# Kernel optimization log

Measured on AMD Instinct MI355X. Metric: run time of the kernel, lower is better.

Reference implementation:

```python
import jax, jax.numpy as jnp
import numpy as np

DIM = 512
HEADS = 8
LANDMARKS = 64


def setup_inputs() -> dict:
    key = jax.random.key(0)
    ks = jax.random.split(key, 9)
    B, N, C = 2, 16384, DIM
    s = 0.02
    return {
        "x": jax.random.normal(ks[0], (B, N, C), dtype=jnp.float32),
        "wq": jax.random.normal(ks[1], (C, C), dtype=jnp.float32) * s,
        "bq": jnp.zeros((C,), dtype=jnp.float32),
        "wk": jax.random.normal(ks[2], (C, C), dtype=jnp.float32) * s,
        "bk": jnp.zeros((C,), dtype=jnp.float32),
        "wv": jax.random.normal(ks[3], (C, C), dtype=jnp.float32) * s,
        "bv": jnp.zeros((C,), dtype=jnp.float32),
        "wo": jax.random.normal(ks[4], (C, C), dtype=jnp.float32) * s,
        "bo": jnp.zeros((C,), dtype=jnp.float32),
    }


def _to_heads(x, H):
    B, N, C = x.shape
    return x.reshape(B, N, H, C // H).transpose(0, 2, 1, 3)  # (B,H,N,hd)


def reference(x, wq, bq, wk, bk, wv, bv, wo, bo):
    B, N, C = x.shape
    H = HEADS
    hd = C // H
    scale = hd ** (-0.5)
    m = min(LANDMARKS, N)

    q = _to_heads(x @ wq.T + bq, H) * scale  # (B,H,N,hd)
    k = _to_heads(x @ wk.T + bk, H)
    v = _to_heads(x @ wv.T + bv, H)

    if N <= m * 2:
        attn = jax.nn.softmax(jnp.einsum("bhnd,bhkd->bhnk", q, k), axis=-1)
        out = jnp.einsum("bhnk,bhkd->bhnd", attn, v)
    else:
        seg = (N + m - 1) // m
        pad = seg * m - N
        if pad > 0:
            q_p = jnp.pad(q, ((0, 0), (0, 0), (0, pad), (0, 0)))
            k_p = jnp.pad(k, ((0, 0), (0, 0), (0, pad), (0, 0)))
        else:
            q_p, k_p = q, k
        # landmarks: mean over consecutive segments of length seg (zero-pad included, as in torch)
        q_land = q_p.reshape(B, H, m, seg, hd).mean(3)  # (B,H,m,hd)
        k_land = k_p.reshape(B, H, m, seg, hd).mean(3)

        ker1 = jax.nn.softmax(jnp.einsum("bhnd,bhmd->bhnm", q, k_land), axis=-1)  # (B,H,N,m)
        ker2 = jax.nn.softmax(jnp.einsum("bhld,bhmd->bhlm", q_land, k_land), axis=-1)  # (B,H,m,m)
        ker3 = jax.nn.softmax(jnp.einsum("bhmd,bhnd->bhmn", q_land, k), axis=-1)  # (B,H,m,N)
        ker2_inv = jnp.linalg.pinv(ker2)  # (B,H,m,m)

        kv = jnp.einsum("bhmn,bhnd->bhmd", ker3, v)  # (B,H,m,hd)
        out = jnp.einsum("bhnm,bhmd->bhnd", ker1, ker2_inv @ kv)

    out = out.transpose(0, 2, 1, 3).reshape(B, N, C)
    return out @ wo.T + bo
```

## Files before the change

### kernel.cpp

```cpp
#include <hip/hip_runtime.h>
#include <stdint.h>


constexpr int B_   = 2;
constexpr int N_   = 16384;
constexpr int C_   = 512;
constexpr int H_   = 8;
constexpr int HD_  = 64;
constexpr int LM_  = 64;
constexpr int SEG_ = 256;
constexpr int BH_  = 16;
constexpr int NCH_ = 16;
constexpr int NPART_ = 64;
constexpr int SW1_ = 4;
constexpr int SW2_ = 1;

#define RCOND_ (640.0 * 1.1920928955078125e-07)

typedef unsigned short ushort4_t __attribute__((ext_vector_type(4)));
typedef unsigned short ushort8_t __attribute__((ext_vector_type(8)));
typedef __bf16 bf16x8 __attribute__((ext_vector_type(8)));
typedef float f32x4 __attribute__((ext_vector_type(4)));

__device__ inline float bf2f(unsigned short u) {
  union { unsigned int i; float f; } x; x.i = ((unsigned int)u) << 16; return x.f;
}
__device__ inline unsigned short f2bf(float f) {
  union { float f; unsigned int i; } x; x.f = f;
  unsigned int lsb = (x.i >> 16) & 1;
  return (unsigned short)((x.i + 0x7fffu + lsb) >> 16);
}
__device__ inline bf16x8 ld_bf8(const unsigned short* p) { return *(const bf16x8*)p; }

__device__ __forceinline__ void gload_lds16(const unsigned short* gsrc, unsigned short* ldst) {
  __builtin_amdgcn_global_load_lds((const __attribute__((address_space(1))) void*)gsrc,
                                   (__attribute__((address_space(3))) void*)ldst, 16, 0, 0);
}

__global__ __launch_bounds__(256) void cvt_w4_kernel(const float* __restrict__ wq,
                                                     const float* __restrict__ wk,
                                                     const float* __restrict__ wv,
                                                     const float* __restrict__ wo,
                                                     unsigned short* __restrict__ dq,
                                                     unsigned short* __restrict__ dk,
                                                     unsigned short* __restrict__ dv,
                                                     unsigned short* __restrict__ dwo) {
  int which = blockIdx.y;
  const float* src = which == 0 ? wq : which == 1 ? wk : which == 2 ? wv : wo;
  unsigned short* dst = which == 0 ? dq : which == 1 ? dk : which == 2 ? dv : dwo;
  int i = blockIdx.x * 256 + threadIdx.x;
  const float* s = src + (size_t)i * 8;
  float4 x0 = *(const float4*)(s);
  float4 x1 = *(const float4*)(s + 4);
  ushort8_t u;
  u[0] = f2bf(x0.x); u[1] = f2bf(x0.y); u[2] = f2bf(x0.z); u[3] = f2bf(x0.w);
  u[4] = f2bf(x1.x); u[5] = f2bf(x1.y); u[6] = f2bf(x1.z); u[7] = f2bf(x1.w);
  *(ushort8_t*)(dst + (size_t)i * 8) = u;
}

__global__ __launch_bounds__(256) void seg_mean_kernel(const float* __restrict__ x,
                                                       float* __restrict__ xbar,
                                                       unsigned short* __restrict__ xb) {
  int bl = blockIdx.x;
  int b = bl / LM_, l = bl % LM_;
  int t = threadIdx.x;
  int c4 = t & 127;
  int rh = t >> 7;
  const size_t rowbase = (size_t)b * N_ + (size_t)l * SEG_;
  const float* xp = x + rowbase * C_;
  float4 s = make_float4(0.f, 0.f, 0.f, 0.f);
  for (int r = rh * 128; r < rh * 128 + 128; ++r) {
    float4 v = *(const float4*)(xp + (size_t)r * C_ + c4 * 4);
    s.x += v.x; s.y += v.y; s.z += v.z; s.w += v.w;
    ushort4_t u;
    u[0] = f2bf(v.x); u[1] = f2bf(v.y); u[2] = f2bf(v.z); u[3] = f2bf(v.w);
    *(ushort4_t*)(xb + (rowbase + r) * C_ + c4 * 4) = u;
  }
  __shared__ float red[2][512];
  *(float4*)&red[rh][c4 * 4] = s;
  __syncthreads();
  if (rh == 0) {
    float4 a = *(float4*)&red[0][c4 * 4];
    float4 c = *(float4*)&red[1][c4 * 4];
    const float invs = 1.0f / SEG_;
    float4 o;
    o.x = (a.x + c.x) * invs; o.y = (a.y + c.y) * invs;
    o.z = (a.z + c.z) * invs; o.w = (a.w + c.w) * invs;
    *(float4*)(xbar + (size_t)bl * C_ + c4 * 4) = o;
  }
}

__global__ __launch_bounds__(256) void land_gemm_kernel(const float* __restrict__ xbar,
                                                        const float* __restrict__ wq,
                                                        const float* __restrict__ bq,
                                                        const float* __restrict__ wk,
                                                        const float* __restrict__ bk,
                                                        float* __restrict__ qland,
                                                        float* __restrict__ kland,
                                                        unsigned short* __restrict__ qlbh,
                                                        unsigned short* __restrict__ qlbl,
                                                        unsigned short* __restrict__ klb) {
  __shared__ float As[32][68];
  __shared__ float Ws[32][68];
  int which = blockIdx.x >> 1;
  int row0 = (blockIdx.x & 1) * 64;
  int col0 = blockIdx.y * 64;
  const float* A = xbar;
  const float* W = which ? wk : wq;
  const float* bias = which ? bk : bq;
  float scale = which ? 1.0f : 0.125f;
  float* out = which ? kland : qland;
  int tid = threadIdx.x;
  int tm = tid >> 4, tn = tid & 15;
  float acc[4][4] = {};
  for (int k0 = 0; k0 < C_; k0 += 32) {
#pragma unroll
    for (int i = 0; i < 2; ++i) {
      int s = tid + i * 256;
      int r = s >> 3;
      int kg = (s & 7) << 2;
      float4 av = *(const float4*)(A + (size_t)(row0 + r) * C_ + k0 + kg);
      As[kg + 0][r] = av.x; As[kg + 1][r] = av.y;
      As[kg + 2][r] = av.z; As[kg + 3][r] = av.w;
      float4 wv = *(const float4*)(W + (size_t)(col0 + r) * C_ + k0 + kg);
      Ws[kg + 0][r] = wv.x; Ws[kg + 1][r] = wv.y;
      Ws[kg + 2][r] = wv.z; Ws[kg + 3][r] = wv.w;
    }
    __syncthreads();
#pragma unroll
    for (int kk = 0; kk < 32; ++kk) {
      float4 a = *(const float4*)&As[kk][tm * 4];
      float4 b = *(const float4*)&Ws[kk][tn * 4];
      float av[4] = {a.x, a.y, a.z, a.w};
      float bv[4] = {b.x, b.y, b.z, b.w};
#pragma unroll
      for (int i = 0; i < 4; ++i)
#pragma unroll
        for (int j = 0; j < 4; ++j) acc[i][j] += av[i] * bv[j];
    }
    __syncthreads();
  }
#pragma unroll
  for (int i = 0; i < 4; ++i) {
    int row = row0 + tm * 4 + i;
    int d0 = tn * 4;
    float o4[4];
#pragma unroll
    for (int j = 0; j < 4; ++j) o4[j] = (acc[i][j] + bias[col0 + d0 + j]) * scale;
    int b = row / LM_, n = row % LM_;
    int h = col0 >> 6;
    size_t idx = (((size_t)(b * H_ + h) * LM_) + n) * HD_ + d0;
    float4 o; o.x = o4[0]; o.y = o4[1]; o.z = o4[2]; o.w = o4[3];
    *(float4*)(out + idx) = o;
    if (which == 0) {
      ushort4_t uh, ul;
#pragma unroll
      for (int j = 0; j < 4; ++j) {
        unsigned short hbits = f2bf(o4[j]);
        uh[j] = hbits;
        ul[j] = f2bf(o4[j] - bf2f(hbits));
      }
      *(ushort4_t*)(qlbh + idx) = uh;
      *(ushort4_t*)(qlbl + idx) = ul;
    } else {
      ushort4_t uk;
#pragma unroll
      for (int j = 0; j < 4; ++j) uk[j] = f2bf(o4[j]);
      *(ushort4_t*)(klb + idx) = uk;
    }
  }
}

__device__ __forceinline__ void dma_gemm_body(const unsigned short* __restrict__ A,
                                              const unsigned short* __restrict__ W,
                                              const float* __restrict__ bias,
                                              void* __restrict__ out,
                                              float scale, int omode,
                                              int row0, int col0,
                                              unsigned short* Xs, unsigned short* Wl,
                                              int tid) {
  int w = tid >> 6, lane = tid & 63;
  int wr = w >> 1, wc = w & 1;
  f32x4 acc[4][4] = {};

  for (int k0 = 0; k0 < C_; k0 += 32) {
    __syncthreads();
#pragma unroll
    for (int i = 0; i < 2; ++i) {
      const unsigned short* gx = A + (size_t)(row0 + w * 32 + i * 16 + (lane >> 2)) * C_ + k0 + (lane & 3) * 8;
      gload_lds16(gx, &Xs[(w * 32 + i * 16) * 32]);
      const unsigned short* gw = W + (size_t)(col0 + w * 32 + i * 16 + (lane >> 2)) * C_ + k0 + (lane & 3) * 8;
      gload_lds16(gw, &Wl[(w * 32 + i * 16) * 32]);
    }
    __syncthreads();
    bf16x8 af[4], bfr[4];
#pragma unroll
    for (int m = 0; m < 4; ++m)
      af[m] = *(bf16x8*)&Xs[(wr * 64 + m * 16 + (lane & 15)) * 32 + (lane >> 4) * 8];
#pragma unroll
    for (int n = 0; n < 4; ++n)
      bfr[n] = *(bf16x8*)&Wl[(wc * 64 + n * 16 + (lane & 15)) * 32 + (lane >> 4) * 8];
#pragma unroll
    for (int m = 0; m < 4; ++m)
#pragma unroll
      for (int n = 0; n < 4; ++n)
        acc[m][n] = __builtin_amdgcn_mfma_f32_16x16x32_bf16(af[m], bfr[n], acc[m][n], 0, 0, 0);
  }

#pragma unroll
  for (int m = 0; m < 4; ++m) {
    int rbase = row0 + wr * 64 + m * 16 + (lane >> 4) * 4;
#pragma unroll
    for (int n = 0; n < 4; ++n) {
      int c = col0 + wc * 64 + n * 16 + (lane & 15);
      float bc = bias[c];
      if (omode == 0) {
#pragma unroll
        for (int rg = 0; rg < 4; ++rg)
          ((float*)out)[(size_t)(rbase + rg) * C_ + c] = acc[m][n][rg] + bc;
      } else if (omode == 2) {
        int b = rbase >> 14, nn = rbase & 16383;
        int h = c >> 6, d = c & 63;
        ushort4_t u;
#pragma unroll
        for (int rg = 0; rg < 4; ++rg) u[rg] = f2bf((acc[m][n][rg] + bc) * scale);
        *(ushort4_t*)((unsigned short*)out + ((size_t)(b * H_ + h) * HD_ + d) * N_ + nn) = u;
      } else {
#pragma unroll
        for (int rg = 0; rg < 4; ++rg) {
          float val = (acc[m][n][rg] + bc) * scale;
          int r = rbase + rg;
          int b = r >> 14, nn = r & 16383, h = c >> 6, d = c & 63;
          ((unsigned short*)out)[(((size_t)(b * H_ + h) * N_) + nn) * HD_ + d] = f2bf(val);
        }
      }
    }
  }
}

template <int NW>
__device__ __forceinline__ void svd_sweeps(float* a, float* v, char* smemraw,
                                           int w, int lane, int nsweeps) {
  constexpr int RP = 64 / NW;
  float (*Ac)[68] = (float(*)[68])(smemraw);
  float (*Vc)[68] = (float(*)[68])(smemraw + 17408);
  float (*pg)[NW][64] = (float(*)[NW][64])(smemraw + 34816);
  float (*pa)[64] = (float(*)[64])(smemraw + 34816 + 2 * NW * 64 * 4);
  const int r0 = w * RP;
#pragma unroll
  for (int c = 0; c < RP; c += 4) {
    *(float4*)&Ac[lane][r0 + c] = make_float4(a[c], a[c + 1], a[c + 2], a[c + 3]);
    *(float4*)&Vc[lane][r0 + c] = make_float4(v[c], v[c + 1], v[c + 2], v[c + 3]);
  }

  for (int sweep = 0; sweep < nsweeps; ++sweep) {
    float p0 = 0.f, p1 = 0.f;
#pragma unroll
    for (int k = 0; k < RP; k += 2) { p0 = fmaf(a[k], a[k], p0); p1 = fmaf(a[k + 1], a[k + 1], p1); }
    pa[w][lane] = p0 + p1;
    __syncthreads();
    float alpha;
    if constexpr (NW == 4)
      alpha = (pa[0][lane] + pa[1][lane]) + (pa[2][lane] + pa[3][lane]);
    else
      alpha = ((pa[0][lane] + pa[1][lane]) + (pa[2][lane] + pa[3][lane])) +
              ((pa[4][lane] + pa[5][lane]) + (pa[6][lane] + pa[7][lane]));
    for (int mask = 1; mask < 64; ++mask) {
      int buf = mask & 1;
      int partner = lane ^ mask;
      bool lower = lane < partner;
      float beta = __shfl_xor(alpha, mask);
      float o[RP];
#pragma unroll
      for (int c = 0; c < RP; c += 4) {
        float4 t4 = *(float4*)&Ac[partner][r0 + c];
        o[c] = t4.x; o[c + 1] = t4.y; o[c + 2] = t4.z; o[c + 3] = t4.w;
      }
      float g0 = 0.f, g1 = 0.f;
#pragma unroll
      for (int k = 0; k < RP; k += 2) { g0 = fmaf(a[k], o[k], g0); g1 = fmaf(a[k + 1], o[k + 1], g1); }
      pg[buf][w][lane] = g0 + g1;
      __syncthreads();
      float gamma;
      if constexpr (NW == 4)
        gamma = (pg[buf][0][lane] + pg[buf][1][lane]) + (pg[buf][2][lane] + pg[buf][3][lane]);
      else
        gamma = ((pg[buf][0][lane] + pg[buf][1][lane]) + (pg[buf][2][lane] + pg[buf][3][lane])) +
                ((pg[buf][4][lane] + pg[buf][5][lane]) + (pg[buf][6][lane] + pg[buf][7][lane]));
      bool need = (gamma * gamma > 1e-12f * alpha * beta);
      if (__any(need)) {
        float ov[RP];
#pragma unroll
        for (int c = 0; c < RP; c += 4) {
          float4 t4 = *(float4*)&Vc[partner][r0 + c];
          ov[c] = t4.x; ov[c + 1] = t4.y; ov[c + 2] = t4.z; ov[c + 3] = t4.w;
        }
        float ap = lower ? alpha : beta;
        float aq = lower ? beta : alpha;
        float c = 1.f, s = 0.f;
        if (need) {
          float tau = (aq - ap) / (2.f * gamma);
          float t = copysignf(1.f, tau) / (fabsf(tau) + sqrtf(fmaf(tau, tau, 1.f)));
          c = rsqrtf(fmaf(t, t, 1.f));
          s = t * c;
        }
        float sm = lower ? -s : s;
#pragma unroll
        for (int k = 0; k < RP; ++k) a[k] = fmaf(sm, o[k], c * a[k]);
#pragma unroll
        for (int k = 0; k < RP; ++k) v[k] = fmaf(sm, ov[k], c * v[k]);
        float twocsg = 2.f * c * s * gamma;
        alpha = fmaf(c * c, alpha, fmaf(s * s, beta, lower ? -twocsg : twocsg));
#pragma unroll
        for (int cc = 0; cc < RP; cc += 4) {
          *(float4*)&Ac[lane][r0 + cc] = make_float4(a[cc], a[cc + 1], a[cc + 2], a[cc + 3]);
          *(float4*)&Vc[lane][r0 + cc] = make_float4(v[cc], v[cc + 1], v[cc + 2], v[cc + 3]);
        }
      }
    }
  }
}

__device__ void svd_phase1(const float* __restrict__ qland, const float* __restrict__ kland,
                           float* __restrict__ asave, float* __restrict__ vsave,
                           int bh, char* smemraw, int tid) {
  __builtin_amdgcn_s_setprio(3);
  float (*qlS)[65] = (float(*)[65])(smemraw);
  float (*klS)[65] = (float(*)[65])(smemraw + 16640);
  for (int i = 0; i < 2; ++i) {
    int s = tid + i * 512;
    int r = s >> 4, d4 = (s & 15) << 2;
    *(float4*)&qlS[r][d4] = *(const float4*)(qland + ((size_t)bh * 64 + r) * 64 + d4);
    *(float4*)&klS[r][d4] = *(const float4*)(kland + ((size_t)bh * 64 + r) * 64 + d4);
  }
  __syncthreads();
  int w = tid >> 6, lane = tid & 63;
  float a[8], v[8];
#pragma unroll
  for (int k = 0; k < 8; ++k) {
    int row = w * 8 + k;
    float acc = 0.f;
#pragma unroll
    for (int d4 = 0; d4 < 64; d4 += 4) {
      float4 qv = *(float4*)&qlS[row][d4];
      float4 kv = *(float4*)&klS[lane][d4];
      acc += qv.x * kv.x + qv.y * kv.y + qv.z * kv.z + qv.w * kv.w;
    }
    float e = expf(acc);
    float rs = e;
#pragma unroll
    for (int m = 1; m < 64; m <<= 1) rs += __shfl_xor(rs, m);
    a[k] = e * (1.f / rs);
  }
#pragma unroll
  for (int k = 0; k < 8; ++k) v[k] = (w * 8 + k == lane) ? 1.f : 0.f;
  __syncthreads();
  svd_sweeps<8>(a, v, smemraw, w, lane, SW1_);
#pragma unroll
  for (int k = 0; k < 8; ++k) {
    asave[((size_t)bh * 64 + w * 8 + k) * 64 + lane] = a[k];
    vsave[((size_t)bh * 64 + w * 8 + k) * 64 + lane] = v[k];
  }
  __builtin_amdgcn_s_setprio(0);
}

__device__ void svd_phase2(const float* __restrict__ asave, const float* __restrict__ vsave,
                           float* __restrict__ pinv, int bh, char* smemraw, int tid) {
  __builtin_amdgcn_s_setprio(3);
  double (*ps2)[64]  = (double(*)[64])(smemraw + 37888);
  float (*vsL)[65]   = (float(*)[65])(smemraw);
  float (*wasL)[65]  = (float(*)[65])(smemraw + 16640);
  int w = tid >> 6, lane = tid & 63;
  float a[16], v[16];
#pragma unroll
  for (int k = 0; k < 16; ++k) {
    a[k] = asave[((size_t)bh * 64 + w * 16 + k) * 64 + lane];
    v[k] = vsave[((size_t)bh * 64 + w * 16 + k) * 64 + lane];
  }
  svd_sweeps<4>(a, v, smemraw, w, lane, SW2_);

  double psig = 0.0;
#pragma unroll
  for (int k = 0; k < 16; ++k) psig += (double)a[k] * (double)a[k];
  ps2[w][lane] = psig;
  __syncthreads();
  double sig2 = (ps2[0][lane] + ps2[1][lane]) + (ps2[2][lane] + ps2[3][lane]);
  double smax = sig2;
#pragma unroll
  for (int m = 1; m < 64; m <<= 1) smax = fmax(smax, __shfl_xor(smax, m));
  double cutoff2 = smax * (RCOND_ * RCOND_);
  float wgt = (sig2 > cutoff2) ? (float)(1.0 / sig2) : 0.f;

#pragma unroll
  for (int k = 0; k < 16; ++k) {
    vsL[lane][w * 16 + k] = v[k];
    wasL[lane][w * 16 + k] = wgt * a[k];
  }
  __syncthreads();
  int i = tid >> 2;
  int j0 = (tid & 3) * 16;
  float acc[16] = {};
  for (int r = 0; r < 64; ++r) {
    float vv = vsL[r][i];
#pragma unroll
    for (int jj = 0; jj < 16; ++jj) acc[jj] = fmaf(vv, wasL[r][j0 + jj], acc[jj]);
  }
#pragma unroll
  for (int jj = 0; jj < 16; jj += 4) {
    float4 ovv = make_float4(acc[jj], acc[jj + 1], acc[jj + 2], acc[jj + 3]);
    *(float4*)(pinv + ((size_t)bh * 64 + i) * 64 + j0 + jj) = ovv;
  }
  __builtin_amdgcn_s_setprio(0);
}

__global__ __launch_bounds__(512) void fused1_kernel(
    const unsigned short* __restrict__ xb,
    const unsigned short* __restrict__ wqb, const float* __restrict__ bq,
    const unsigned short* __restrict__ wkb, const float* __restrict__ bk,
    const unsigned short* __restrict__ wvb, const float* __restrict__ bv,
    unsigned short* __restrict__ q4, unsigned short* __restrict__ k4,
    unsigned short* __restrict__ vt,
    const float* __restrict__ qland, const float* __restrict__ kland,
    float* __restrict__ asave, float* __restrict__ vsave) {
  __shared__ __align__(16) char smem[40960];
  int tid = threadIdx.x;
  int blk = blockIdx.x;
  if (blk < 16) { svd_phase1(qland, kland, asave, vsave, blk, smem, tid); return; }
  int g = blk - 16;
  int which = g >> 9;
  int subpair = g & 511;
  int half = tid >> 8;
  int ltid = tid & 255;
  int sub = subpair * 2 + half;
  int row0 = (sub >> 2) * 128;
  int col0 = (sub & 3) * 128;
  unsigned short* Xs = (unsigned short*)(smem + half * 16384);
  unsigned short* Wl = Xs + 128 * 32;
  if (which == 0)
    dma_gemm_body(xb, wqb, bq, q4, 0.125f, 1, row0, col0, Xs, Wl, ltid);
  else if (which == 1)
    dma_gemm_body(xb, wkb, bk, k4, 1.0f, 1, row0, col0, Xs, Wl, ltid);
  else
    dma_gemm_body(xb, wvb, bv, vt, 1.0f, 2, row0, col0, Xs, Wl, ltid);
}

__device__ void ker3kv_body(const unsigned short* __restrict__ qlh,
                            const unsigned short* __restrict__ qll,
                            const unsigned short* __restrict__ k4,
                            const unsigned short* __restrict__ vt,
                            float* __restrict__ pacc,
                            float* __restrict__ pacc0,
                            float* __restrict__ ps,
                            int bh, int ch, char* smemraw, int tid) {
  int w = tid >> 6, lane = tid & 63;
  int part = ch * 4 + w;
  int lrow = lane & 15, lgrp = lane >> 4;
  unsigned short* myP = (unsigned short*)smemraw + w * 64 * 72;

  bf16x8 qah[4][2], qal[4][2];
#pragma unroll
  for (int mf = 0; mf < 4; ++mf)
#pragma unroll
    for (int ks = 0; ks < 2; ++ks) {
      size_t off = ((size_t)bh * 64 + mf * 16 + lrow) * 64 + ks * 32 + lgrp * 8;
      qah[mf][ks] = ld_bf8(qlh + off);
      qal[mf][ks] = ld_bf8(qll + off);
    }
  bf16x8 onesf;
#pragma unroll
  for (int j = 0; j < 8; ++j) onesf[j] = (__bf16)1.0f;

  f32x4 kvacc[4][4] = {};
  f32x4 oneacc[4] = {};
  f32x4 ssum[4] = {};

  for (int sub = 0; sub < 4; ++sub) {
    int n0 = ch * 1024 + w * 256 + sub * 64;
    f32x4 sacc[4][4] = {};
#pragma unroll
    for (int ks = 0; ks < 2; ++ks) {
#pragma unroll
      for (int nf = 0; nf < 4; ++nf) {
        bf16x8 kb = ld_bf8(k4 + ((size_t)bh * N_ + n0 + nf * 16 + lrow) * 64 + ks * 32 + lgrp * 8);
#pragma unroll
        for (int mf = 0; mf < 4; ++mf) {
          sacc[mf][nf] = __builtin_amdgcn_mfma_f32_16x16x32_bf16(qah[mf][ks], kb, sacc[mf][nf], 0, 0, 0);
          sacc[mf][nf] = __builtin_amdgcn_mfma_f32_16x16x32_bf16(qal[mf][ks], kb, sacc[mf][nf], 0, 0, 0);
        }
      }
    }
#pragma unroll
    for (int mf = 0; mf < 4; ++mf) {
#pragma unroll
      for (int nf = 0; nf < 4; ++nf) {
#pragma unroll
        for (int r = 0; r < 4; ++r) {
          float pd = expf(sacc[mf][nf][r]) - 1.0f;
          ssum[mf][r] += pd;
          myP[(mf * 16 + lgrp * 4 + r) * 72 + nf * 16 + lrow] = f2bf(pd);
        }
      }
    }
#pragma unroll
    for (int ks = 0; ks < 2; ++ks) {
      bf16x8 pa[4];
#pragma unroll
      for (int mf = 0; mf < 4; ++mf)
        pa[mf] = ld_bf8(myP + (mf * 16 + lrow) * 72 + ks * 32 + lgrp * 8);
#pragma unroll
      for (int nf = 0; nf < 4; ++nf) {
        bf16x8 vb = ld_bf8(vt + ((size_t)bh * 64 + nf * 16 + lrow) * N_ + n0 + ks * 32 + lgrp * 8);
#pragma unroll
        for (int mf = 0; mf < 4; ++mf)
          kvacc[mf][nf] = __builtin_amdgcn_mfma_f32_16x16x32_bf16(pa[mf], vb, kvacc[mf][nf], 0, 0, 0);
        oneacc[nf] = __builtin_amdgcn_mfma_f32_16x16x32_bf16(onesf, vb, oneacc[nf], 0, 0, 0);
      }
    }
  }
#pragma unroll
  for (int mf = 0; mf < 4; ++mf)
#pragma unroll
    for (int m = 1; m < 16; m <<= 1)
#pragma unroll
      for (int r = 0; r < 4; ++r) ssum[mf][r] += __shfl_xor(ssum[mf][r], m);

  size_t pb = (((size_t)bh * NPART_ + part) * 64) * 64;
#pragma unroll
  for (int mf = 0; mf < 4; ++mf)
#pragma unroll
    for (int nf = 0; nf < 4; ++nf)
#pragma unroll
      for (int r = 0; r < 4; ++r)
        pacc[pb + (size_t)(mf * 16 + lgrp * 4 + r) * 64 + nf * 16 + lrow] = kvacc[mf][nf][r];
  if (lrow == 0) {
#pragma unroll
    for (int mf = 0; mf < 4; ++mf)
#pragma unroll
      for (int r = 0; r < 4; ++r)
        ps[((size_t)bh * NPART_ + part) * 64 + mf * 16 + lgrp * 4 + r] = ssum[mf][r];
  }
  if (lgrp == 0) {
#pragma unroll
    for (int nf = 0; nf < 4; ++nf)
      pacc0[((size_t)bh * NPART_ + part) * 64 + nf * 16 + lrow] = oneacc[nf][0];
  }
}

__global__ __launch_bounds__(256, 1) void fused2_kernel(
    const unsigned short* __restrict__ qlh,
    const unsigned short* __restrict__ qll,
    const unsigned short* __restrict__ k4,
    const unsigned short* __restrict__ vt,
    float* __restrict__ pacc, float* __restrict__ pacc0, float* __restrict__ ps,
    const float* __restrict__ asave, const float* __restrict__ vsave,
    float* __restrict__ pinv) {
  __shared__ __align__(16) char smem[39936];
  int tid = threadIdx.x;
  int blk = blockIdx.x;
  if (blk < 16) { svd_phase2(asave, vsave, pinv, blk, smem, tid); return; }
  int g = blk - 16;
  int bh = g >> 4, ch = g & 15;
  ker3kv_body(qlh, qll, k4, vt, pacc, pacc0, ps, bh, ch, smem, tid);
}

__global__ __launch_bounds__(256) void cm_kernel(const float* __restrict__ pacc,
                                                 const float* __restrict__ pacc0,
                                                 const float* __restrict__ ps,
                                                 const float* __restrict__ pinv,
                                                 unsigned short* __restrict__ mtbh,
                                                 unsigned short* __restrict__ mtbl,
                                                 float* __restrict__ msum) {
  int bh = blockIdx.x;
  int tid = threadIdx.x;
  __shared__ float kvs[64][68];
  __shared__ double pcsd[64];
  for (int g = 0; g < 4; ++g) {
    int lm = g * 16 + (tid >> 4);
    int d4 = (tid & 15) * 4;
    float s = 16384.f;
    for (int part = 0; part < NPART_; ++part) s += ps[((size_t)bh * NPART_ + part) * 64 + lm];
    float4 a = make_float4(0.f, 0.f, 0.f, 0.f);
    for (int part = 0; part < NPART_; ++part) {
      float4 c0 = *(const float4*)&pacc0[((size_t)bh * NPART_ + part) * 64 + d4];
      float4 v = *(const float4*)&pacc[(((size_t)bh * NPART_ + part) * 64 + lm) * 64 + d4];
      a.x += c0.x + v.x; a.y += c0.y + v.y; a.z += c0.z + v.z; a.w += c0.w + v.w;
    }
    float inv = 1.f / s;
    kvs[lm][d4 + 0] = a.x * inv; kvs[lm][d4 + 1] = a.y * inv;
    kvs[lm][d4 + 2] = a.z * inv; kvs[lm][d4 + 3] = a.w * inv;
  }
  if (tid < 64) {
    double s = 0.0;
    for (int l = 0; l < 64; ++l) s += (double)pinv[((size_t)bh * 64 + l) * 64 + tid];
    pcsd[tid] = s;
  }
  __syncthreads();
  int l = tid >> 2, t = tid & 3;
  double o[16] = {};
  for (int j = 0; j < 64; ++j) {
    double pv = (double)pinv[((size_t)bh * 64 + l) * 64 + j];
#pragma unroll
    for (int i = 0; i < 16; ++i) o[i] += pv * (double)kvs[j][t * 16 + i];
  }
#pragma unroll
  for (int i = 0; i < 16; ++i) {
    float f = (float)o[i];
    unsigned short hi = f2bf(f);
    float lo = f - bf2f(hi);
    int d = t * 16 + i;
    mtbh[((size_t)bh * 64 + d) * 64 + l] = hi;
    mtbl[((size_t)bh * 64 + d) * 64 + l] = f2bf(lo);
  }
  if (tid < 64) {
    double m = 0.0;
    for (int j = 0; j < 64; ++j) m += pcsd[j] * (double)kvs[j][tid];
    msum[(size_t)bh * 64 + tid] = (float)(m * (1.0 / 64.0));
  }
}

__global__ __launch_bounds__(256, 1) void ker1out_mfma_kernel(
    const unsigned short* __restrict__ q4,
    const unsigned short* __restrict__ klb,
    const unsigned short* __restrict__ mtbh,
    const unsigned short* __restrict__ mtbl,
    const float* __restrict__ msum,
    unsigned short* __restrict__ outh) {
  int bh = blockIdx.y, tile = blockIdx.x;
  int b = bh >> 3, h = bh & 7;
  int tid = threadIdx.x, w = tid >> 6, lane = tid & 63;
  int lrow = lane & 15, lgrp = lane >> 4;
  int tok0 = tile * 256 + w * 64;
  __shared__ __align__(16) unsigned short Pl[4][64 * 72];
  unsigned short* myP = &Pl[w][0];

  f32x4 sacc[4][4] = {};
#pragma unroll
  for (int ks = 0; ks < 2; ++ks) {
    bf16x8 kb[4];
#pragma unroll
    for (int nf = 0; nf < 4; ++nf)
      kb[nf] = ld_bf8(klb + ((size_t)bh * 64 + nf * 16 + lrow) * 64 + ks * 32 + lgrp * 8);
#pragma unroll
    for (int mf = 0; mf < 4; ++mf) {
      bf16x8 qa = ld_bf8(q4 + ((size_t)bh * N_ + tok0 + mf * 16 + lrow) * 64 + ks * 32 + lgrp * 8);
#pragma unroll
      for (int nf = 0; nf < 4; ++nf)
        sacc[mf][nf] = __builtin_amdgcn_mfma_f32_16x16x32_bf16(qa, kb[nf], sacc[mf][nf], 0, 0, 0);
    }
  }
  f32x4 ssum[4] = {};
#pragma unroll
  for (int mf = 0; mf < 4; ++mf)
#pragma unroll
    for (int nf = 0; nf < 4; ++nf)
#pragma unroll
      for (int r = 0; r < 4; ++r) {
        sacc[mf][nf][r] = expf(sacc[mf][nf][r]);
        ssum[mf][r] += sacc[mf][nf][r];
      }
#pragma unroll
  for (int mf = 0; mf < 4; ++mf)
#pragma unroll
    for (int m = 1; m < 16; m <<= 1)
#pragma unroll
      for (int r = 0; r < 4; ++r) ssum[mf][r] += __shfl_xor(ssum[mf][r], m);
#pragma unroll
  for (int mf = 0; mf < 4; ++mf) {
    f32x4 inv;
#pragma unroll
    for (int r = 0; r < 4; ++r) inv[r] = 1.f / ssum[mf][r];
#pragma unroll
    for (int nf = 0; nf < 4; ++nf)
#pragma unroll
      for (int r = 0; r < 4; ++r) {
        float pdev = fmaf(sacc[mf][nf][r], inv[r], -0.015625f);
        myP[(mf * 16 + lgrp * 4 + r) * 72 + nf * 16 + lrow] = f2bf(pdev);
      }
  }

  f32x4 oacc[4][4] = {};
#pragma unroll
  for (int ks = 0; ks < 2; ++ks) {
    bf16x8 pa[4];
#pragma unroll
    for (int mf = 0; mf < 4; ++mf)
      pa[mf] = ld_bf8(myP + (mf * 16 + lrow) * 72 + ks * 32 + lgrp * 8);
#pragma unroll
    for (int nf = 0; nf < 4; ++nf) {
      bf16x8 mh = ld_bf8(mtbh + ((size_t)bh * 64 + nf * 16 + lrow) * 64 + ks * 32 + lgrp * 8);
      bf16x8 ml = ld_bf8(mtbl + ((size_t)bh * 64 + nf * 16 + lrow) * 64 + ks * 32 + lgrp * 8);
#pragma unroll
      for (int mf = 0; mf < 4; ++mf) {
        oacc[mf][nf] = __builtin_amdgcn_mfma_f32_16x16x32_bf16(pa[mf], mh, oacc[mf][nf], 0, 0, 0);
        oacc[mf][nf] = __builtin_amdgcn_mfma_f32_16x16x32_bf16(pa[mf], ml, oacc[mf][nf], 0, 0, 0);
      }
    }
  }
#pragma unroll
  for (int nf = 0; nf < 4; ++nf) {
    float ms = msum[(size_t)bh * 64 + nf * 16 + lrow];
#pragma unroll
    for (int mf = 0; mf < 4; ++mf)
#pragma unroll
      for (int r = 0; r < 4; ++r) {
        int tok = tok0 + mf * 16 + lgrp * 4 + r;
        int d = nf * 16 + lrow;
        outh[((size_t)b * N_ + tok) * C_ + h * HD_ + d] = f2bf(oacc[mf][nf][r] + ms);
      }
  }
}

__global__ __launch_bounds__(256) void oproj_kernel(const unsigned short* __restrict__ outh,
                                                    const unsigned short* __restrict__ wob,
                                                    const float* __restrict__ bo,
                                                    float* __restrict__ out) {
  __shared__ __align__(16) unsigned short Xs[128 * 32];
  __shared__ __align__(16) unsigned short Wl[128 * 32];
  dma_gemm_body(outh, wob, bo, out, 1.0f, 0, blockIdx.x * 128, blockIdx.y * 128,
                Xs, Wl, threadIdx.x);
}

extern "C" void kernel_launch(void* const* d_in, const int* in_sizes, int n_in,
                              void* d_out, int out_size, void* d_ws, size_t ws_size,
                              hipStream_t stream) {
  const float* x  = (const float*)d_in[0];
  const float* wq = (const float*)d_in[1];
  const float* bq = (const float*)d_in[2];
  const float* wk = (const float*)d_in[3];
  const float* bk = (const float*)d_in[4];
  const float* wv = (const float*)d_in[5];
  const float* bv = (const float*)d_in[6];
  const float* wo = (const float*)d_in[7];
  const float* bo = (const float*)d_in[8];
  float* out = (float*)d_out;

  char* base = (char*)d_ws;
  const size_t QKV = (size_t)BH_ * N_ * HD_;
  unsigned short* q4 = (unsigned short*)base;
  unsigned short* k4 = (unsigned short*)(base + QKV * 2);
  unsigned short* vt = (unsigned short*)(base + QKV * 4);
  unsigned short* outh = (unsigned short*)(base + QKV * 2);
  char* sp = base + QKV * 6;
  float* pacc  = (float*)sp; sp += (size_t)BH_ * NPART_ * 64 * 64 * 4;
  float* pacc0 = (float*)sp; sp += (size_t)BH_ * NPART_ * 64 * 4;
  float* ps    = (float*)sp; sp += (size_t)BH_ * NPART_ * 64 * 4;
  float* xbar  = (float*)sp; sp += (size_t)B_ * LM_ * C_ * 4;
  float* qland = (float*)sp; sp += (size_t)BH_ * LM_ * HD_ * 4;
  float* kland = (float*)sp; sp += (size_t)BH_ * LM_ * HD_ * 4;
  unsigned short* qlbh = (unsigned short*)sp; sp += (size_t)BH_ * LM_ * HD_ * 2;
  unsigned short* qlbl = (unsigned short*)sp; sp += (size_t)BH_ * LM_ * HD_ * 2;
  unsigned short* klb  = (unsigned short*)sp; sp += (size_t)BH_ * LM_ * HD_ * 2;
  float* pinv  = (float*)sp; sp += (size_t)BH_ * LM_ * LM_ * 4;
  unsigned short* mtbh = (unsigned short*)sp; sp += (size_t)BH_ * LM_ * HD_ * 2;
  unsigned short* mtbl = (unsigned short*)sp; sp += (size_t)BH_ * LM_ * HD_ * 2;
  float* msum  = (float*)sp; sp += (size_t)BH_ * HD_ * 4;
  float* asave = (float*)sp; sp += (size_t)BH_ * LM_ * LM_ * 4;
  float* vsave = (float*)sp; sp += (size_t)BH_ * LM_ * LM_ * 4;
  unsigned short* wob = (unsigned short*)sp; sp += (size_t)C_ * C_ * 2;
  unsigned short* wqb = (unsigned short*)sp; sp += (size_t)C_ * C_ * 2;
  unsigned short* wkb = (unsigned short*)sp; sp += (size_t)C_ * C_ * 2;
  unsigned short* wvb = (unsigned short*)sp; sp += (size_t)C_ * C_ * 2;

  unsigned short* xb = (unsigned short*)d_out;

  const int W8 = (C_ * C_) / 8;

  dim3 gc(W8 / 256, 4);
  cvt_w4_kernel<<<gc, 256, 0, stream>>>(wq, wk, wv, wo, wqb, wkb, wvb, wob);

  seg_mean_kernel<<<B_ * LM_, 256, 0, stream>>>(x, xbar, xb);
  dim3 gl(4, 8);
  land_gemm_kernel<<<gl, 256, 0, stream>>>(xbar, wq, bq, wk, bk,
                                           qland, kland, qlbh, qlbl, klb);

  fused1_kernel<<<16 + 3 * 512, 512, 0, stream>>>(
      xb, wqb, bq, wkb, bk, wvb, bv, q4, k4, vt, qland, kland, asave, vsave);

  fused2_kernel<<<16 + NCH_ * BH_, 256, 0, stream>>>(
      qlbh, qlbl, k4, vt, pacc, pacc0, ps, asave, vsave, pinv);

  cm_kernel<<<BH_, 256, 0, stream>>>(pacc, pacc0, ps, pinv, mtbh, mtbl, msum);

  dim3 g9(N_ / 256, BH_);
  ker1out_mfma_kernel<<<g9, 256, 0, stream>>>(q4, klb, mtbh, mtbl, msum, outh);

  dim3 g10(B_ * N_ / 128, C_ / 128);
  oproj_kernel<<<g10, 256, 0, stream>>>(outh, wob, bo, out);
}
```

Baseline: 448.5 us.

## Widen seg-mean and fused2 blocks to 512 threads, rebalance SVD sweeps

The segment-mean kernel now uses 512 threads, with four row-quarters reduced through shared memory instead of two halves. fused2 runs 512-thread blocks: the SVD phase-2 blocks use 8 waves holding 8 rows each, and ker3kv blocks each handle two chunks, one per 256-thread half, with separate shared-memory regions. The Jacobi SVD sweep split moves from 4+1 to 3+2, shifting work from the fused1 phase into the wider fused2 phase. The goal is to shorten the serial SVD critical path and cut block count. The cost is more shared memory per block and possible occupancy changes.

```diff
diff --git a/kernel.cpp b/kernel.cpp
--- a/kernel.cpp
+++ b/kernel.cpp
@@ -12,8 +12,8 @@
 constexpr int BH_  = 16;
 constexpr int NCH_ = 16;
 constexpr int NPART_ = 64;
-constexpr int SW1_ = 4;
-constexpr int SW2_ = 1;
+constexpr int SW1_ = 3;
+constexpr int SW2_ = 2;
 
 #define RCOND_ (640.0 * 1.1920928955078125e-07)
 
@@ -58,34 +58,38 @@
   *(ushort8_t*)(dst + (size_t)i * 8) = u;
 }
 
-__global__ __launch_bounds__(256) void seg_mean_kernel(const float* __restrict__ x,
+__global__ __launch_bounds__(512) void seg_mean_kernel(const float* __restrict__ x,
                                                        float* __restrict__ xbar,
                                                        unsigned short* __restrict__ xb) {
   int bl = blockIdx.x;
   int b = bl / LM_, l = bl % LM_;
   int t = threadIdx.x;
   int c4 = t & 127;
-  int rh = t >> 7;
+  int rq = t >> 7;
   const size_t rowbase = (size_t)b * N_ + (size_t)l * SEG_;
   const float* xp = x + rowbase * C_;
   float4 s = make_float4(0.f, 0.f, 0.f, 0.f);
-  for (int r = rh * 128; r < rh * 128 + 128; ++r) {
+  for (int r = rq * 64; r < rq * 64 + 64; ++r) {
     float4 v = *(const float4*)(xp + (size_t)r * C_ + c4 * 4);
     s.x += v.x; s.y += v.y; s.z += v.z; s.w += v.w;
     ushort4_t u;
     u[0] = f2bf(v.x); u[1] = f2bf(v.y); u[2] = f2bf(v.z); u[3] = f2bf(v.w);
     *(ushort4_t*)(xb + (rowbase + r) * C_ + c4 * 4) = u;
   }
-  __shared__ float red[2][512];
-  *(float4*)&red[rh][c4 * 4] = s;
+  __shared__ float red[4][512];
+  *(float4*)&red[rq][c4 * 4] = s;
   __syncthreads();
-  if (rh == 0) {
-    float4 a = *(float4*)&red[0][c4 * 4];
-    float4 c = *(float4*)&red[1][c4 * 4];
+  if (rq == 0) {
+    float4 a0 = *(float4*)&red[0][c4 * 4];
+    float4 a1 = *(float4*)&red[1][c4 * 4];
+    float4 a2 = *(float4*)&red[2][c4 * 4];
+    float4 a3 = *(float4*)&red[3][c4 * 4];
     const float invs = 1.0f / SEG_;
     float4 o;
-    o.x = (a.x + c.x) * invs; o.y = (a.y + c.y) * invs;
-    o.z = (a.z + c.z) * invs; o.w = (a.w + c.w) * invs;
+    o.x = ((a0.x + a1.x) + (a2.x + a3.x)) * invs;
+    o.y = ((a0.y + a1.y) + (a2.y + a3.y)) * invs;
+    o.z = ((a0.z + a1.z) + (a2.z + a3.z)) * invs;
+    o.w = ((a0.w + a1.w) + (a2.w + a3.w)) * invs;
     *(float4*)(xbar + (size_t)bl * C_ + c4 * 4) = o;
   }
 }
@@ -367,24 +371,25 @@
 __device__ void svd_phase2(const float* __restrict__ asave, const float* __restrict__ vsave,
                            float* __restrict__ pinv, int bh, char* smemraw, int tid) {
   __builtin_amdgcn_s_setprio(3);
-  double (*ps2)[64]  = (double(*)[64])(smemraw + 37888);
+  double (*ps2)[64]  = (double(*)[64])(smemraw + 40960);
   float (*vsL)[65]   = (float(*)[65])(smemraw);
   float (*wasL)[65]  = (float(*)[65])(smemraw + 16640);
   int w = tid >> 6, lane = tid & 63;
-  float a[16], v[16];
-#pragma unroll
-  for (int k = 0; k < 16; ++k) {
-    a[k] = asave[((size_t)bh * 64 + w * 16 + k) * 64 + lane];
-    v[k] = vsave[((size_t)bh * 64 + w * 16 + k) * 64 + lane];
-  }
-  svd_sweeps<4>(a, v, smemraw, w, lane, SW2_);
+  float a[8], v[8];
+#pragma unroll
+  for (int k = 0; k < 8; ++k) {
+    a[k] = asave[((size_t)bh * 64 + w * 8 + k) * 64 + lane];
+    v[k] = vsave[((size_t)bh * 64 + w * 8 + k) * 64 + lane];
+  }
+  svd_sweeps<8>(a, v, smemraw, w, lane, SW2_);
 
   double psig = 0.0;
 #pragma unroll
-  for (int k = 0; k < 16; ++k) psig += (double)a[k] * (double)a[k];
+  for (int k = 0; k < 8; ++k) psig += (double)a[k] * (double)a[k];
   ps2[w][lane] = psig;
   __syncthreads();
-  double sig2 = (ps2[0][lane] + ps2[1][lane]) + (ps2[2][lane] + ps2[3][lane]);
+  double sig2 = ((ps2[0][lane] + ps2[1][lane]) + (ps2[2][lane] + ps2[3][lane])) +
+                ((ps2[4][lane] + ps2[5][lane]) + (ps2[6][lane] + ps2[7][lane]));
   double smax = sig2;
 #pragma unroll
   for (int m = 1; m < 64; m <<= 1) smax = fmax(smax, __shfl_xor(smax, m));
@@ -392,21 +397,21 @@
   float wgt = (sig2 > cutoff2) ? (float)(1.0 / sig2) : 0.f;
 
 #pragma unroll
-  for (int k = 0; k < 16; ++k) {
-    vsL[lane][w * 16 + k] = v[k];
-    wasL[lane][w * 16 + k] = wgt * a[k];
+  for (int k = 0; k < 8; ++k) {
+    vsL[lane][w * 8 + k] = v[k];
+    wasL[lane][w * 8 + k] = wgt * a[k];
   }
   __syncthreads();
-  int i = tid >> 2;
-  int j0 = (tid & 3) * 16;
-  float acc[16] = {};
+  int i = tid >> 3;
+  int j0 = (tid & 7) * 8;
+  float acc[8] = {};
   for (int r = 0; r < 64; ++r) {
     float vv = vsL[r][i];
 #pragma unroll
-    for (int jj = 0; jj < 16; ++jj) acc[jj] = fmaf(vv, wasL[r][j0 + jj], acc[jj]);
-  }
-#pragma unroll
-  for (int jj = 0; jj < 16; jj += 4) {
+    for (int jj = 0; jj < 8; ++jj) acc[jj] = fmaf(vv, wasL[r][j0 + jj], acc[jj]);
+  }
+#pragma unroll
+  for (int jj = 0; jj < 8; jj += 4) {
     float4 ovv = make_float4(acc[jj], acc[jj + 1], acc[jj + 2], acc[jj + 3]);
     *(float4*)(pinv + ((size_t)bh * 64 + i) * 64 + j0 + jj) = ovv;
   }
@@ -546,7 +551,7 @@
   }
 }
 
-__global__ __launch_bounds__(256, 1) void fused2_kernel(
+__global__ __launch_bounds__(512, 1) void fused2_kernel(
     const unsigned short* __restrict__ qlh,
     const unsigned short* __restrict__ qll,
     const unsigned short* __restrict__ k4,
@@ -554,13 +559,16 @@
     float* __restrict__ pacc, float* __restrict__ pacc0, float* __restrict__ ps,
     const float* __restrict__ asave, const float* __restrict__ vsave,
     float* __restrict__ pinv) {
-  __shared__ __align__(16) char smem[39936];
+  __shared__ __align__(16) char smem[73728];
   int tid = threadIdx.x;
   int blk = blockIdx.x;
   if (blk < 16) { svd_phase2(asave, vsave, pinv, blk, smem, tid); return; }
   int g = blk - 16;
-  int bh = g >> 4, ch = g & 15;
-  ker3kv_body(qlh, qll, k4, vt, pacc, pacc0, ps, bh, ch, smem, tid);
+  int bh = g >> 3, cpair = g & 7;
+  int half = tid >> 8;
+  int ltid = tid & 255;
+  int ch = cpair * 2 + half;
+  ker3kv_body(qlh, qll, k4, vt, pacc, pacc0, ps, bh, ch, smem + half * 36864, ltid);
 }
 
 __global__ __launch_bounds__(256) void cm_kernel(const float* __restrict__ pacc,
@@ -768,7 +776,7 @@
   dim3 gc(W8 / 256, 4);
   cvt_w4_kernel<<<gc, 256, 0, stream>>>(wq, wk, wv, wo, wqb, wkb, wvb, wob);
 
-  seg_mean_kernel<<<B_ * LM_, 256, 0, stream>>>(x, xbar, xb);
+  seg_mean_kernel<<<B_ * LM_, 512, 0, stream>>>(x, xbar, xb);
   dim3 gl(4, 8);
   land_gemm_kernel<<<gl, 256, 0, stream>>>(xbar, wq, bq, wk, bk,
                                            qland, kland, qlbh, qlbl, klb);
@@ -776,7 +784,7 @@
   fused1_kernel<<<16 + 3 * 512, 512, 0, stream>>>(
       xb, wqb, bq, wkb, bk, wvb, bv, q4, k4, vt, qland, kland, asave, vsave);
 
-  fused2_kernel<<<16 + NCH_ * BH_, 256, 0, stream>>>(
+  fused2_kernel<<<16 + BH_ * 8, 512, 0, stream>>>(
       qlbh, qlbl, k4, vt, pacc, pacc0, ps, asave, vsave, pinv);
 
   cm_kernel<<<BH_, 256, 0, stream>>>(pacc, pacc0, ps, pinv, mtbh, mtbl, msum);
```

New measurement: 392.2 us. -12.5%, faster.
